# Kernel tuning notes

Hardware: AMD Instinct MI355X
Metric: run time of the kernel (lower is better)

The kernel has to match this reference:

```python
import jax, jax.numpy as jnp
import numpy as np

B, S, E, H = 4, 1024, 1024, 16
HD = E // H  # head_dim = 64
MAX_SEQ = 1024  # rel positions span [-(MAX_SEQ-1), MAX_SEQ-1]


def setup_inputs() -> dict:
    key = jax.random.key(0)
    ks = jax.random.split(key, 12)
    std_e = 1.0 / np.sqrt(E)
    std_h = 1.0 / np.sqrt(HD)
    inp = {
        "x": jax.random.normal(ks[0], (B, S, E), dtype=jnp.float32),
        # torch nn.Linear weights are [out, in]; y = x @ W.T + b
        "Wq": jax.random.uniform(ks[1], (E, E), jnp.float32, -std_e, std_e),
        "bq": jax.random.uniform(ks[2], (E,), jnp.float32, -std_e, std_e),
        "Wk": jax.random.uniform(ks[3], (E, E), jnp.float32, -std_e, std_e),
        "bk": jax.random.uniform(ks[4], (E,), jnp.float32, -std_e, std_e),
        "Wv": jax.random.uniform(ks[5], (E, E), jnp.float32, -std_e, std_e),
        "bv": jax.random.uniform(ks[6], (E,), jnp.float32, -std_e, std_e),
        "Wo": jax.random.uniform(ks[7], (E, E), jnp.float32, -std_e, std_e),
        "bo": jax.random.uniform(ks[8], (E,), jnp.float32, -std_e, std_e),
        # pos_key_proj: Linear(head_dim, head_dim, bias=False)
        "Wp": jax.random.uniform(ks[9], (HD, HD), jnp.float32, -std_h, std_h),
        # learned relative position table [2*max_seq_len-1, head_dim]
        "rel_table": jax.random.normal(ks[10], (2 * MAX_SEQ - 1, HD), dtype=jnp.float32),
    }
    return inp


def _rel_shift(pos_scores):
    # pos_scores: [B, H, S, 2S-1] -> [B, H, S, S]
    # result[..., i, j] = pos_scores[..., i, (S-1) - i + j]
    s = pos_scores.shape[-2]
    idx = (s - 1) - jnp.arange(s)[:, None] + jnp.arange(s)[None, :]  # [S, S]
    return jnp.take_along_axis(pos_scores, idx[None, None, :, :], axis=-1)


def reference(x, Wq, bq, Wk, bk, Wv, bv, Wo, bo, Wp, rel_table):
    scale = 1.0 / np.sqrt(HD)
    Q = (x @ Wq.T + bq).reshape(B, S, H, HD).transpose(0, 2, 1, 3)  # [B,H,S,HD]
    K = (x @ Wk.T + bk).reshape(B, S, H, HD).transpose(0, 2, 1, 3)
    V = (x @ Wv.T + bv).reshape(B, S, H, HD).transpose(0, 2, 1, 3)

    # rel_pos_encoding(S): slice centered at MAX_SEQ-1 covering 2S-1 positions
    center = MAX_SEQ - 1
    rel_emb = rel_table[center - (S - 1): center + S]  # [2S-1, HD]
    rel_key = rel_emb @ Wp.T                            # [2S-1, HD]

    content = jnp.einsum("bhqd,bhkd->bhqk", Q, K) * scale       # [B,H,S,S]
    pos = jnp.einsum("bhqd,pd->bhqp", Q, rel_key) * scale       # [B,H,S,2S-1]
    scores = content + _rel_shift(pos)                          # [B,H,S,S]

    probs = jax.nn.softmax(scores, axis=-1)
    ctx = jnp.einsum("bhqk,bhkd->bhqd", probs, V)               # [B,H,S,HD]
    ctx = ctx.transpose(0, 2, 1, 3).reshape(B, S, E)
    return ctx @ Wo.T + bo
```

## Files before the change

### kernel.cpp

```cpp
#include <hip/hip_runtime.h>
#include <hip/hip_bf16.h>

#define B_   4
#define S_   1024
#define E_   1024
#define H_   16
#define HD_  64

typedef float  f32x4  __attribute__((ext_vector_type(4)));
typedef short  bf16x8 __attribute__((ext_vector_type(8)));
typedef short  bf16x4 __attribute__((ext_vector_type(4)));

__device__ __forceinline__ float bf2f(short u) {
  union { unsigned int i; float f; } v;
  v.i = ((unsigned int)(unsigned short)u) << 16;
  return v.f;
}
__device__ __forceinline__ short f2bf(float f) {
  unsigned int x = __float_as_uint(f);
  x = x + 0x7fffu + ((x >> 16) & 1u);
  return (short)(x >> 16);
}
__device__ __forceinline__ bf16x8 ld_cvt8(const float* __restrict__ p) {
  const f32x4 a = *(const f32x4*)p;
  const f32x4 b = *(const f32x4*)(p + 4);
  bf16x8 r;
  r[0] = f2bf(a[0]); r[1] = f2bf(a[1]); r[2] = f2bf(a[2]); r[3] = f2bf(a[3]);
  r[4] = f2bf(b[0]); r[5] = f2bf(b[1]); r[6] = f2bf(b[2]); r[7] = f2bf(b[3]);
  return r;
}

__device__ __forceinline__ void gload_lds16(const short* g, short* l) {
  __builtin_amdgcn_global_load_lds(
      (const __attribute__((address_space(1))) void*)g,
      (__attribute__((address_space(3))) void*)l, 16, 0, 0);
}

__global__ __launch_bounds__(256) void cvt_f32_bf16(
    const float* __restrict__ src, short* __restrict__ dst, int n)
{
  const int i = (blockIdx.x * 256 + threadIdx.x) * 4;
  if (i < n) {
    const f32x4 v = *(const f32x4*)(src + i);
    bf16x4 o;
    o[0] = f2bf(v[0]); o[1] = f2bf(v[1]); o[2] = f2bf(v[2]); o[3] = f2bf(v[3]);
    *(bf16x4*)(dst + i) = o;
  }
}

__global__ __launch_bounds__(256) void cvt7_f32_bf16(
    const float* __restrict__ w0, const float* __restrict__ w1,
    const float* __restrict__ w2, const float* __restrict__ x,
    short* __restrict__ WB, short* __restrict__ xbf)
{
  const int NW = E_ * E_;
  const int y = blockIdx.y;
  const float* src;
  short* dst;
  if (y < 3) { src = (y == 0) ? w0 : (y == 1) ? w1 : w2; dst = WB + (size_t)y * NW; }
  else       { src = x + (size_t)(y - 3) * NW;           dst = xbf + (size_t)(y - 3) * NW; }
  const int i = (blockIdx.x * 256 + threadIdx.x) * 4;
  const f32x4 v = *(const f32x4*)(src + i);
  bf16x4 o;
  o[0] = f2bf(v[0]); o[1] = f2bf(v[1]); o[2] = f2bf(v[2]); o[3] = f2bf(v[3]);
  *(bf16x4*)(dst + i) = o;
}

template<int TM, int OUTF32>
__global__ __launch_bounds__(256) void gemm_bt(
    const short* __restrict__ A,
    const short* __restrict__ W0, const short* __restrict__ W1, const short* __restrict__ W2,
    const float* __restrict__ b0, const float* __restrict__ b1, const float* __restrict__ b2,
    void* __restrict__ C0v, void* __restrict__ C1v, void* __restrict__ C2v, int vz)
{
  constexpr int NJ = (TM == 128) ? 4 : 2;
  __shared__ short As[TM * 32];
  __shared__ short Bs[128 * 32];

  const int tid  = threadIdx.x;
  const int lane = tid & 63;
  const int wave = tid >> 6;
  const int quad = lane >> 4;
  const int l15  = lane & 15;
  const int wmb  = (TM == 128) ? (wave >> 1) * 64 : 0;
  const int wnb  = (TM == 128) ? (wave & 1) * 64 : wave * 32;
  const int m0   = blockIdx.y * TM;
  const int n0   = blockIdx.x * 128;
  const int z    = blockIdx.z;

  const short* W  = (z == 0) ? W0 : (z == 1) ? W1 : W2;
  const float* bb = (z == 0) ? b0 : (z == 1) ? b1 : b2;
  void*        Cv = (z == 0) ? C0v : (z == 1) ? C1v : C2v;

  const int trow = tid >> 2;
  const int tc   = tid & 3;

  f32x4 acc[4][NJ] = {};

  for (int k0 = 0; k0 < E_; k0 += 32) {
#pragma unroll
    for (int n = 0; n < TM / 64; ++n) {
      const int row  = trow + n * 64;
      const int srcc = tc ^ ((row >> 1) & 3);
      gload_lds16(A + (size_t)(m0 + row) * E_ + k0 + srcc * 8, &As[n * 2048 + tid * 8]);
    }
#pragma unroll
    for (int n = 0; n < 2; ++n) {
      const int row  = trow + n * 64;
      const int srcc = tc ^ ((row >> 1) & 3);
      gload_lds16(W + (size_t)(n0 + row) * E_ + k0 + srcc * 8, &Bs[n * 2048 + tid * 8]);
    }
    __syncthreads();

    bf16x8 af[4], bfr[NJ];
#pragma unroll
    for (int i = 0; i < 4; ++i) {
      const int row = wmb + i * 16 + l15;
      const int pc  = quad ^ ((row >> 1) & 3);
      af[i] = *(bf16x8*)&As[row * 32 + pc * 8];
    }
#pragma unroll
    for (int j = 0; j < NJ; ++j) {
      const int row = wnb + j * 16 + l15;
      const int pc  = quad ^ ((row >> 1) & 3);
      bfr[j] = *(bf16x8*)&Bs[row * 32 + pc * 8];
    }
#pragma unroll
    for (int i = 0; i < 4; ++i)
#pragma unroll
      for (int j = 0; j < NJ; ++j)
        acc[i][j] = __builtin_amdgcn_mfma_f32_16x16x32_bf16(af[i], bfr[j], acc[i][j], 0, 0, 0);
    __syncthreads();
  }

  if (TM == 128 && z == vz) {
    const int mtb = m0 + wmb;
    const int bq  = mtb >> 10;
    const int kt  = (mtb >> 6) & 15;
    short* Cs = (short*)Cv;
#pragma unroll
    for (int j = 0; j < NJ; ++j) {
      const int n = n0 + wnb + j * 16 + l15;
      const float bv = bb[n];
      const int h = (n >> 6) & 15;
      const int d = n & 63;
      bf16x8 lo, hi;
#pragma unroll
      for (int e = 0; e < 8; ++e) {
        lo[e] = f2bf(acc[e & 3][j][e >> 2] + bv);
        hi[e] = f2bf(acc[e & 3][j][(e >> 2) + 2] + bv);
      }
      const size_t off = ((size_t)((bq * 16 + h) * 64 + d)) * 1024 + kt * 64 + quad * 16;
      *(bf16x8*)(Cs + off)     = lo;
      *(bf16x8*)(Cs + off + 8) = hi;
    }
  } else {
#pragma unroll
    for (int j = 0; j < NJ; ++j) {
      const int n = n0 + wnb + j * 16 + l15;
      const float bv = bb[n];
#pragma unroll
      for (int i = 0; i < 4; ++i) {
        const int m = m0 + wmb + i * 16 + quad * 4;
#pragma unroll
        for (int r = 0; r < 4; ++r) {
          const float v = acc[i][j][r] + bv;
          if (OUTF32) ((float*)Cv)[(size_t)(m + r) * E_ + n] = v;
          else        ((short*)Cv)[(size_t)(m + r) * E_ + n] = f2bf(v);
        }
      }
    }
  }
}

__global__ __launch_bounds__(256) void relkey_mfma(
    const float* __restrict__ rel, const float* __restrict__ Wp, short* __restrict__ RKw)
{
  const int tid  = threadIdx.x;
  const int lane = tid & 63;
  const int wv   = tid >> 6;
  const int quad = lane >> 4;
  const int l15  = lane & 15;
  const int p0   = blockIdx.x * 64 + wv * 16;

  bf16x8 af[2];
  {
    int prow = p0 + l15; if (prow > 2046) prow = 2046;
    const float* ap = rel + (size_t)prow * 64 + quad * 8;
    af[0] = ld_cvt8(ap);
    af[1] = ld_cvt8(ap + 32);
  }
  f32x4 acc[4] = {};
#pragma unroll
  for (int nt = 0; nt < 4; ++nt) {
    const float* bp = Wp + (size_t)(nt * 16 + l15) * 64 + quad * 8;
    acc[nt] = __builtin_amdgcn_mfma_f32_16x16x32_bf16(af[0], ld_cvt8(bp),      acc[nt], 0, 0, 0);
    acc[nt] = __builtin_amdgcn_mfma_f32_16x16x32_bf16(af[1], ld_cvt8(bp + 32), acc[nt], 0, 0, 0);
  }
#pragma unroll
  for (int r = 0; r < 4; ++r) {
    const int p = p0 + quad * 4 + r;
    if (p < 2047)
#pragma unroll
      for (int nt = 0; nt < 4; ++nt)
        RKw[(size_t)p * 64 + nt * 16 + l15] = f2bf(acc[nt][r]);
  }
}

__global__ __launch_bounds__(512, 4) void attn_kernel(
    const short* __restrict__ Qw, const short* __restrict__ Kw,
    const short* __restrict__ Vtg, const short* __restrict__ RKw,
    short* __restrict__ Cw)
{
  __shared__ short Ks[64][72];
  __shared__ short Vt[64][72];
  __shared__ short RKs[192][72];
  __shared__ short Ps[8][16][72];

  const int tid  = threadIdx.x;
  const int lane = tid & 63;
  const int wv   = tid >> 6;
  const int quad = lane >> 4;
  const int l15  = lane & 15;

  const int lid  = blockIdx.x;
  const int pair = (lid & 7) * 8 + (lid >> 6);
  const int qt   = (lid >> 3) & 7;
  const int b    = pair >> 4;
  const int h    = pair & 15;
  const int bh   = pair;
  const int q0   = qt * 128;
  const int qw0  = q0 + wv * 16;
  const int jb   = 112 - 16 * wv;
  const int pbase0 = S_ - 128 - q0;

  bf16x8 qf[2];
  {
    const size_t base = (size_t)(b * S_ + qw0 + l15) * E_ + h * HD_ + quad * 8;
    qf[0] = *(const bf16x8*)(Qw + base);
    qf[1] = *(const bf16x8*)(Qw + base + 32);
  }

  f32x4 oacc[4] = {};
  float lsum[4] = {0.f, 0.f, 0.f, 0.f};

  const float fs = 0.125f * 1.44269504088896340736f;

  const int sr  = tid >> 3;
  const int sc8 = (tid & 7) * 8;

#pragma unroll 1
  for (int kt = 0; kt < 16; ++kt) {
    const int k0 = kt * 64;

    *(bf16x8*)&Ks[sr][sc8] =
        *(const bf16x8*)(Kw + (size_t)(b * S_ + k0 + sr) * E_ + h * HD_ + sc8);
    *(bf16x8*)&Vt[sr][sc8] =
        *(const bf16x8*)(Vtg + (size_t)(bh * 64 + sr) * 1024 + k0 + sc8);
    if (kt == 0) {
#pragma unroll
      for (int jj = 0; jj < 3; ++jj) {
        const int c = tid + jj * 512;
        const int row = c >> 3, ch = (c & 7) * 8;
        int p = pbase0 + row; p = (p > 2046) ? 2046 : p;
        *(bf16x8*)&RKs[row][ch] = *(const bf16x8*)(RKw + (size_t)p * 64 + ch);
      }
    } else {
      const int phys0 = 64 * ((kt + 2) % 3);
      int p = pbase0 + 64 * kt + 128 + sr; p = (p > 2046) ? 2046 : p;
      *(bf16x8*)&RKs[phys0 + sr][sc8] = *(const bf16x8*)(RKw + (size_t)p * 64 + sc8);
    }
    __syncthreads();

    const int s64 = 64 * (kt % 3);

    f32x4 sc[4] = {};
#pragma unroll
    for (int s = 0; s < 2; ++s) {
#pragma unroll
      for (int kk = 0; kk < 4; ++kk) {
        bf16x8 bf = *(bf16x8*)&Ks[kk*16 + l15][s*32 + quad*8];
        sc[kk] = __builtin_amdgcn_mfma_f32_16x16x32_bf16(qf[s], bf, sc[kk], 0, 0, 0);
      }
    }

    f32x4 ta[5] = {};
#pragma unroll
    for (int jt = 0; jt < 5; ++jt) {
      int phys = s64 + jb + jt * 16;
      if (phys >= 192) phys -= 192;
#pragma unroll
      for (int s = 0; s < 2; ++s) {
        bf16x8 bf = *(bf16x8*)&RKs[phys + l15][s*32 + quad*8];
        ta[jt] = __builtin_amdgcn_mfma_f32_16x16x32_bf16(qf[s], bf, ta[jt], 0, 0, 0);
      }
    }

    float p[4][4];
#pragma unroll
    for (int r = 0; r < 4; ++r) {
      const int i16 = quad*4 + r;
      const int d   = 15 + l15 - i16;
      const int srcLane = (quad << 4) | (d & 15);
      float sj[5];
#pragma unroll
      for (int jt = 0; jt < 5; ++jt) sj[jt] = __shfl(ta[jt][r], srcLane, 64);
      const bool hi = (d >= 16);
#pragma unroll
      for (int kk = 0; kk < 4; ++kk) {
        const float t = hi ? sj[kk+1] : sj[kk];
        const float sv = fminf((sc[kk][r] + t) * fs, 108.f);
        const float pv = exp2f(sv - 12.f);
        p[kk][r] = pv;
        lsum[r] += pv;
      }
    }

#pragma unroll
    for (int r = 0; r < 4; ++r) {
      bf16x4 pw;
      pw[0] = f2bf(p[0][r]); pw[1] = f2bf(p[1][r]);
      pw[2] = f2bf(p[2][r]); pw[3] = f2bf(p[3][r]);
      *(bf16x4*)&Ps[wv][quad*4 + r][l15*4] = pw;
    }

#pragma unroll
    for (int ks = 0; ks < 2; ++ks) {
      bf16x8 pa = *(bf16x8*)&Ps[wv][l15][ks*32 + quad*8];
#pragma unroll
      for (int dt = 0; dt < 4; ++dt) {
        bf16x8 vb = *(bf16x8*)&Vt[dt*16 + l15][ks*32 + quad*8];
        oacc[dt] = __builtin_amdgcn_mfma_f32_16x16x32_bf16(pa, vb, oacc[dt], 0, 0, 0);
      }
    }
    __syncthreads();
  }

#pragma unroll
  for (int off = 1; off <= 8; off <<= 1)
#pragma unroll
    for (int r = 0; r < 4; ++r)
      lsum[r] += __shfl_xor(lsum[r], off, 64);

#pragma unroll
  for (int r = 0; r < 4; ++r) {
    const float inv = 1.0f / lsum[r];
    const size_t row = (size_t)(b * S_ + qw0 + quad*4 + r) * E_ + h * HD_;
#pragma unroll
    for (int dt = 0; dt < 4; ++dt)
      Cw[row + dt*16 + l15] = f2bf(oacc[dt][r] * inv);
  }
}

__global__ void fill_kernel(float* __restrict__ out, int n, float val) {
  for (int i = blockIdx.x * blockDim.x + threadIdx.x; i < n; i += gridDim.x * blockDim.x)
    out[i] = val;
}

extern "C" void kernel_launch(void* const* d_in, const int* in_sizes, int n_in,
                              void* d_out, int out_size, void* d_ws, size_t ws_size,
                              hipStream_t stream)
{
  const size_t WS_NEEDED = 33816448;
  if (ws_size < WS_NEEDED) {
    fill_kernel<<<1024, 256, 0, stream>>>((float*)d_out, out_size, 0.25f);
    return;
  }
  if (n_in != 11 || in_sizes[10] != 2047 * 64) {
    fill_kernel<<<1024, 256, 0, stream>>>((float*)d_out, out_size, 0.75f);
    return;
  }

  const float* x   = (const float*)d_in[0];
  const float* Wq  = (const float*)d_in[1];
  const float* bq  = (const float*)d_in[2];
  const float* Wk  = (const float*)d_in[3];
  const float* bk  = (const float*)d_in[4];
  const float* Wv  = (const float*)d_in[5];
  const float* bv  = (const float*)d_in[6];
  const float* Wo  = (const float*)d_in[7];
  const float* bo  = (const float*)d_in[8];
  const float* Wp  = (const float*)d_in[9];
  const float* rel = (const float*)d_in[10];

  char* ws = (char*)d_ws;
  short* Qws = (short*)(ws);
  short* Kws = (short*)(ws + 8388608);
  short* Vtg = (short*)(ws + 16777216);
  short* WB  = (short*)(ws + 25165824);
  short* ctx = (short*)(ws + 25165824);
  short* WoB = (short*)(ws + 8388608);
  short* RKw = (short*)(ws + 33554432);
  short* xbf = (short*)d_out;

  const int NW = E_ * E_;

  cvt7_f32_bf16<<<dim3(1024, 7), dim3(256), 0, stream>>>(Wq, Wk, Wv, x, WB, xbf);

  gemm_bt<128, 0><<<dim3(8, 32, 3), dim3(256), 0, stream>>>(
      xbf, WB, WB + NW, WB + 2 * NW, bq, bk, bv, Qws, Kws, Vtg, 2);

  relkey_mfma<<<dim3(32), dim3(256), 0, stream>>>(rel, Wp, RKw);

  attn_kernel<<<dim3(512), dim3(512), 0, stream>>>(Qws, Kws, Vtg, RKw, ctx);

  cvt_f32_bf16<<<dim3(NW / 1024), dim3(256), 0, stream>>>(Wo, WoB, NW);

  gemm_bt<64, 1><<<dim3(8, 64, 1), dim3(256), 0, stream>>>(
      ctx, WoB, WoB, WoB, bo, bo, bo, d_out, d_out, d_out, -1);
}
```

Baseline: 273.3 us.

## Shrink attention blocks to 64 queries and read rel-keys directly from global

The attention kernel now uses 256-thread blocks covering 64 query rows, launching 1024 blocks instead of 512. It drops the shared-memory ring buffer for relative-position keys, and each wave loads its needed RK fragments straight from global memory into registers. This cuts shared memory use and per-block work, which may allow more resident blocks and shorter tail effects. In exchange, K/V tiles are reloaded by twice as many blocks and RK reads become uncoalesced per-wave global loads with no sharing across waves.

```diff
diff --git a/kernel.cpp b/kernel.cpp
--- a/kernel.cpp
+++ b/kernel.cpp
@@ -207,15 +207,14 @@
   }
 }
 
-__global__ __launch_bounds__(512, 4) void attn_kernel(
+__global__ __launch_bounds__(256, 3) void attn_kernel(
     const short* __restrict__ Qw, const short* __restrict__ Kw,
     const short* __restrict__ Vtg, const short* __restrict__ RKw,
     short* __restrict__ Cw)
 {
   __shared__ short Ks[64][72];
   __shared__ short Vt[64][72];
-  __shared__ short RKs[192][72];
-  __shared__ short Ps[8][16][72];
+  __shared__ short Ps[4][16][72];
 
   const int tid  = threadIdx.x;
   const int lane = tid & 63;
@@ -224,15 +223,16 @@
   const int l15  = lane & 15;
 
   const int lid  = blockIdx.x;
-  const int pair = (lid & 7) * 8 + (lid >> 6);
-  const int qt   = (lid >> 3) & 7;
+  const int idx  = lid >> 3;
+  const int pair = (lid & 7) * 8 + (idx >> 4);
+  const int qt   = idx & 15;
   const int b    = pair >> 4;
   const int h    = pair & 15;
   const int bh   = pair;
-  const int q0   = qt * 128;
+  const int q0   = qt * 64;
   const int qw0  = q0 + wv * 16;
-  const int jb   = 112 - 16 * wv;
-  const int pbase0 = S_ - 128 - q0;
+  const int jb   = 48 - 16 * wv;
+  const int pbase0 = S_ - 64 - q0;
 
   bf16x8 qf[2];
   {
@@ -255,24 +255,25 @@
 
     *(bf16x8*)&Ks[sr][sc8] =
         *(const bf16x8*)(Kw + (size_t)(b * S_ + k0 + sr) * E_ + h * HD_ + sc8);
+    *(bf16x8*)&Ks[sr + 32][sc8] =
+        *(const bf16x8*)(Kw + (size_t)(b * S_ + k0 + sr + 32) * E_ + h * HD_ + sc8);
     *(bf16x8*)&Vt[sr][sc8] =
         *(const bf16x8*)(Vtg + (size_t)(bh * 64 + sr) * 1024 + k0 + sc8);
-    if (kt == 0) {
-#pragma unroll
-      for (int jj = 0; jj < 3; ++jj) {
-        const int c = tid + jj * 512;
-        const int row = c >> 3, ch = (c & 7) * 8;
-        int p = pbase0 + row; p = (p > 2046) ? 2046 : p;
-        *(bf16x8*)&RKs[row][ch] = *(const bf16x8*)(RKw + (size_t)p * 64 + ch);
-      }
-    } else {
-      const int phys0 = 64 * ((kt + 2) % 3);
-      int p = pbase0 + 64 * kt + 128 + sr; p = (p > 2046) ? 2046 : p;
-      *(bf16x8*)&RKs[phys0 + sr][sc8] = *(const bf16x8*)(RKw + (size_t)p * 64 + sc8);
-    }
+    *(bf16x8*)&Vt[sr + 32][sc8] =
+        *(const bf16x8*)(Vtg + (size_t)(bh * 64 + sr + 32) * 1024 + k0 + sc8);
     __syncthreads();
 
-    const int s64 = 64 * (kt % 3);
+    bf16x8 rkb[5][2];
+    {
+      const int pb = pbase0 + 64 * kt + jb + l15;
+#pragma unroll
+      for (int jt = 0; jt < 5; ++jt) {
+        int p = pb + jt * 16; if (p > 2046) p = 2046;
+        const short* rp = RKw + (size_t)p * 64 + quad * 8;
+        rkb[jt][0] = *(const bf16x8*)rp;
+        rkb[jt][1] = *(const bf16x8*)(rp + 32);
+      }
+    }
 
     f32x4 sc[4] = {};
 #pragma unroll
@@ -287,13 +288,8 @@
     f32x4 ta[5] = {};
 #pragma unroll
     for (int jt = 0; jt < 5; ++jt) {
-      int phys = s64 + jb + jt * 16;
-      if (phys >= 192) phys -= 192;
-#pragma unroll
-      for (int s = 0; s < 2; ++s) {
-        bf16x8 bf = *(bf16x8*)&RKs[phys + l15][s*32 + quad*8];
-        ta[jt] = __builtin_amdgcn_mfma_f32_16x16x32_bf16(qf[s], bf, ta[jt], 0, 0, 0);
-      }
+      ta[jt] = __builtin_amdgcn_mfma_f32_16x16x32_bf16(qf[0], rkb[jt][0], ta[jt], 0, 0, 0);
+      ta[jt] = __builtin_amdgcn_mfma_f32_16x16x32_bf16(qf[1], rkb[jt][1], ta[jt], 0, 0, 0);
     }
 
     float p[4][4];
@@ -402,7 +398,7 @@
 
   relkey_mfma<<<dim3(32), dim3(256), 0, stream>>>(rel, Wp, RKw);
 
-  attn_kernel<<<dim3(512), dim3(512), 0, stream>>>(Qws, Kws, Vtg, RKw, ctx);
+  attn_kernel<<<dim3(1024), dim3(256), 0, stream>>>(Qws, Kws, Vtg, RKw, ctx);
 
   cvt_f32_bf16<<<dim3(NW / 1024), dim3(256), 0, stream>>>(Wo, WoB, NW);
 
```

Result: slower. 302.9 us (+10.8%).

## Prefetch next K/V/rel-key tiles into registers to overlap global loads with compute

Applied to the files above, without the earlier changes.

Moves the first tile loads before the loop and, each iteration, issues the global loads for the next K, V and rel-key tiles into registers before the MFMA work. After compute, it syncs and writes them into shared memory. The rel-key ring buffer grows from three to four 64-row slots so the prefetched slot never aliases rows still being read. The aim is to hide global load latency behind the score and PV MFMAs, at the cost of extra registers and shared memory, which may reduce occupancy.

```diff
diff --git a/kernel.cpp b/kernel.cpp
--- a/kernel.cpp
+++ b/kernel.cpp
@@ -214,7 +214,7 @@
 {
   __shared__ short Ks[64][72];
   __shared__ short Vt[64][72];
-  __shared__ short RKs[192][72];
+  __shared__ short RKs[256][72];
   __shared__ short Ps[8][16][72];
 
   const int tid  = threadIdx.x;
@@ -249,30 +249,34 @@
   const int sr  = tid >> 3;
   const int sc8 = (tid & 7) * 8;
 
+  {
+    *(bf16x8*)&Ks[sr][sc8] =
+        *(const bf16x8*)(Kw + (size_t)(b * S_ + sr) * E_ + h * HD_ + sc8);
+    *(bf16x8*)&Vt[sr][sc8] =
+        *(const bf16x8*)(Vtg + (size_t)(bh * 64 + sr) * 1024 + sc8);
+#pragma unroll
+    for (int jj = 0; jj < 3; ++jj) {
+      const int c = tid + jj * 512;
+      const int row = c >> 3, ch = (c & 7) * 8;
+      int p = pbase0 + row; p = (p > 2046) ? 2046 : p;
+      *(bf16x8*)&RKs[row][ch] = *(const bf16x8*)(RKw + (size_t)p * 64 + ch);
+    }
+    __syncthreads();
+  }
+
 #pragma unroll 1
   for (int kt = 0; kt < 16; ++kt) {
-    const int k0 = kt * 64;
-
-    *(bf16x8*)&Ks[sr][sc8] =
-        *(const bf16x8*)(Kw + (size_t)(b * S_ + k0 + sr) * E_ + h * HD_ + sc8);
-    *(bf16x8*)&Vt[sr][sc8] =
-        *(const bf16x8*)(Vtg + (size_t)(bh * 64 + sr) * 1024 + k0 + sc8);
-    if (kt == 0) {
-#pragma unroll
-      for (int jj = 0; jj < 3; ++jj) {
-        const int c = tid + jj * 512;
-        const int row = c >> 3, ch = (c & 7) * 8;
-        int p = pbase0 + row; p = (p > 2046) ? 2046 : p;
-        *(bf16x8*)&RKs[row][ch] = *(const bf16x8*)(RKw + (size_t)p * 64 + ch);
-      }
-    } else {
-      const int phys0 = 64 * ((kt + 2) % 3);
-      int p = pbase0 + 64 * kt + 128 + sr; p = (p > 2046) ? 2046 : p;
-      *(bf16x8*)&RKs[phys0 + sr][sc8] = *(const bf16x8*)(RKw + (size_t)p * 64 + sc8);
-    }
-    __syncthreads();
-
-    const int s64 = 64 * (kt % 3);
+    bf16x8 kreg, vreg, rkreg;
+    const bool havekv = (kt < 15);
+    const bool haverk = (kt < 15);
+    if (havekv) {
+      kreg = *(const bf16x8*)(Kw + (size_t)(b * S_ + (kt + 1) * 64 + sr) * E_ + h * HD_ + sc8);
+      vreg = *(const bf16x8*)(Vtg + (size_t)(bh * 64 + sr) * 1024 + (kt + 1) * 64 + sc8);
+    }
+    if (haverk) {
+      int p = pbase0 + 64 * (kt + 3) + sr; if (p > 2046) p = 2046;
+      rkreg = *(const bf16x8*)(RKw + (size_t)p * 64 + sc8);
+    }
 
     f32x4 sc[4] = {};
 #pragma unroll
@@ -287,11 +291,12 @@
     f32x4 ta[5] = {};
 #pragma unroll
     for (int jt = 0; jt < 5; ++jt) {
-      int phys = s64 + jb + jt * 16;
-      if (phys >= 192) phys -= 192;
+      const int off  = jb + jt * 16;
+      const int slot = (kt + (off >> 6)) & 3;
+      const int prow = slot * 64 + (off & 63);
 #pragma unroll
       for (int s = 0; s < 2; ++s) {
-        bf16x8 bf = *(bf16x8*)&RKs[phys + l15][s*32 + quad*8];
+        bf16x8 bf = *(bf16x8*)&RKs[prow + l15][s*32 + quad*8];
         ta[jt] = __builtin_amdgcn_mfma_f32_16x16x32_bf16(qf[s], bf, ta[jt], 0, 0, 0);
       }
     }
@@ -332,6 +337,15 @@
         bf16x8 vb = *(bf16x8*)&Vt[dt*16 + l15][ks*32 + quad*8];
         oacc[dt] = __builtin_amdgcn_mfma_f32_16x16x32_bf16(pa, vb, oacc[dt], 0, 0, 0);
       }
+    }
+
+    __syncthreads();
+    if (havekv) {
+      *(bf16x8*)&Ks[sr][sc8] = kreg;
+      *(bf16x8*)&Vt[sr][sc8] = vreg;
+    }
+    if (haverk) {
+      *(bf16x8*)&RKs[((kt + 3) & 3) * 64 + sr][sc8] = rkreg;
     }
     __syncthreads();
   }
```

New measurement: 256.6 us. 1.07x faster.
